# Kernel optimization log

Hardware: AMD Instinct MI355X
Metric: run time of the kernel (lower is better)

The kernel has to match this reference:

```python
import jax, jax.numpy as jnp
import numpy as np

B, T, S = 32, 32, 400
H, E = 512, 300
V, MAX_OOV = 45000, 50
EXT_V = V + MAX_OOV
NEG = 1.0e12  # INF constant from the torch module


def setup_inputs() -> dict:
    key = jax.random.key(0)
    ks = jax.random.split(key, 16)
    p = lambda k, shape: jax.random.normal(k, shape, jnp.float32) * 0.02
    ext = jax.random.randint(ks[0], (B, S), 0, EXT_V, dtype=jnp.int64 if jax.config.jax_enable_x64 else jnp.int32)
    ext = ext.at[0, 0].set(EXT_V - 1)  # pin max OOV id so num_oov == MAX_OOV (matches torch data-dependent size)
    return {
        "trg_seq_embedded": jax.random.normal(ks[1], (B, T, E), jnp.float32),
        "ext_src_seq": ext,
        "init_states": jax.random.normal(ks[2], (1, B, H), jnp.float32),
        "encoder_outputs": jax.random.normal(ks[3], (B, S, H), jnp.float32),
        "encoder_mask": jnp.ones((B, S), jnp.int32),
        "W_enc": p(ks[4], (H, H)), "b_enc": jnp.zeros((H,), jnp.float32),
        "W_red": p(ks[5], (E, E + H)), "b_red": jnp.zeros((E,), jnp.float32),
        "W_ih": p(ks[6], (4 * H, E)), "W_hh": p(ks[7], (4 * H, H)),
        "b_ih": jnp.zeros((4 * H,), jnp.float32), "b_hh": jnp.zeros((4 * H,), jnp.float32),
        "W_cat": p(ks[8], (H, 2 * H)), "b_cat": jnp.zeros((H,), jnp.float32),
        "W_log": p(ks[9], (V, H)), "b_log": jnp.zeros((V,), jnp.float32),
    }


def reference(trg_seq_embedded, ext_src_seq, init_states, encoder_outputs, encoder_mask,
              W_enc, b_enc, W_red, b_red, W_ih, W_hh, b_ih, b_hh, W_cat, b_cat, W_log, b_log):
    batch = trg_seq_embedded.shape[0]
    # encoder features (memories): [B, S, H]
    memories = jnp.einsum('bsh,gh->bsg', encoder_outputs, W_enc) + b_enc
    batch_idx = jnp.arange(batch)[:, None]
    bias = b_ih + b_hh

    def step(carry, emb):
        h, c, ctx, cov = carry
        # reduce_layer on [embedded ; prev_context] -> [B, E]
        x = jnp.concatenate([emb, ctx], axis=-1) @ W_red.T + b_red
        # single-layer LSTM cell, torch gate order i,f,g,o
        gates = x @ W_ih.T + h @ W_hh.T + bias
        i_g, f_g, g_g, o_g = jnp.split(gates, 4, axis=-1)
        c_new = jax.nn.sigmoid(f_g) * c + jax.nn.sigmoid(i_g) * jnp.tanh(g_g)
        h_new = jax.nn.sigmoid(o_g) * jnp.tanh(c_new)
        # Bahdanau-style dot attention
        energy = jnp.einsum('bh,bsh->bs', h_new, memories)
        energy = jnp.where(encoder_mask == 0, -NEG, energy)
        attn = jax.nn.softmax(energy, axis=1)
        context = jnp.einsum('bs,bsh->bh', attn, memories)
        # output projection
        logit_in = jnp.tanh(jnp.concatenate([h_new, context], axis=-1) @ W_cat.T + b_cat)
        logit = logit_in @ W_log.T + b_log  # [B, V]
        # pointer: scatter_max of energies into extended vocabulary
        ext_logit = jnp.concatenate([logit, jnp.zeros((batch, EXT_V - V), logit.dtype)], axis=1)
        out = jnp.full((batch, EXT_V), -NEG, logit.dtype).at[batch_idx, ext_src_seq].max(energy)
        out = jnp.where(out == -NEG, 0.0, out)
        logit2 = ext_logit + out
        logit2 = jnp.where(logit2 == 0.0, -NEG, logit2)
        return (h_new, c_new, context, cov + attn), (logit2, attn, cov, energy)

    h0 = init_states[0]
    carry0 = (h0, h0, jnp.zeros((batch, memories.shape[-1]), trg_seq_embedded.dtype),
              jnp.zeros((batch, memories.shape[1]), trg_seq_embedded.dtype))
    _, (logits, attn_out, cov_out, energies) = jax.lax.scan(
        step, carry0, jnp.swapaxes(trg_seq_embedded, 0, 1))
    # each stacked over time: logits [T,B,EXT_V], attn/coverage/energies [T,B,S]
    return logits, attn_out, cov_out, energies
```

## Files before the change

kernel.cpp:

```cpp
#include <hip/hip_runtime.h>
#include <hip/hip_bf16.h>

typedef _Float16 h2 __attribute__((ext_vector_type(2)));
typedef _Float16 h8 __attribute__((ext_vector_type(8)));
typedef __attribute__((ext_vector_type(4))) float floatx4;

#define NEGF 1.0e12f

#if __has_builtin(__builtin_amdgcn_fdot2)
#define DOT2(a,b,c) __builtin_amdgcn_fdot2((a),(b),(c),false)
#else
static __device__ __forceinline__ float DOT2(h2 a, h2 b, float c){
  return c + (float)a[0]*(float)b[0] + (float)a[1]*(float)b[1];
}
#endif

__device__ __forceinline__ float dot8(h8 a, h8 b, float c){
  h2 a0 = {a[0],a[1]}, a1 = {a[2],a[3]}, a2 = {a[4],a[5]}, a3 = {a[6],a[7]};
  h2 b0 = {b[0],b[1]}, b1 = {b[2],b[3]}, b2 = {b[4],b[5]}, b3 = {b[6],b[7]};
  c = DOT2(a0,b0,c); c = DOT2(a1,b1,c); c = DOT2(a2,b2,c); c = DOT2(a3,b3,c);
  return c;
}

__device__ __forceinline__ unsigned f16bits(float x){
  union { _Float16 h; unsigned short u; } cv; cv.h = (_Float16)x; return (unsigned)cv.u;
}

#define GLD_LDS16(g, l) __builtin_amdgcn_global_load_lds( \
    (const __attribute__((address_space(1))) void*)(g),   \
    (__attribute__((address_space(3))) void*)(l), 16, 0, 0)

#define ALOAD64(p)    __hip_atomic_load((p), __ATOMIC_RELAXED, __HIP_MEMORY_SCOPE_AGENT)
#define ALOAD32(p)    __hip_atomic_load((p), __ATOMIC_RELAXED, __HIP_MEMORY_SCOPE_AGENT)
#define ASTORE32(p,v) __hip_atomic_store((p), (v), __ATOMIC_RELAXED, __HIP_MEMORY_SCOPE_AGENT)

template<int EPI>
__global__ __launch_bounds__(256) void gemm_f16(
    const _Float16* __restrict__ A, const _Float16* __restrict__ B,
    float* __restrict__ Cf, _Float16* __restrict__ Ch,
    const float* __restrict__ bias, int N, int K, int ldc, int ntn)
{
  __shared__ char smem[32768];
  _Float16* Al = (_Float16*)smem;
  _Float16* Bl = (_Float16*)(smem + 16384);
  int bid = blockIdx.x;
  int bn = bid % ntn, bm = bid / ntn;
  int t = threadIdx.x;
  int w = t >> 6, l = t & 63;

  floatx4 acc[4][4];
#pragma unroll
  for (int i = 0; i < 4; ++i)
#pragma unroll
    for (int j = 0; j < 4; ++j) acc[i][j] = (floatx4){0.f, 0.f, 0.f, 0.f};

  const char* Ab = (const char*)A + (size_t)bm * 128 * K * 2;
  const char* Bb = (const char*)B + (size_t)bn * 128 * K * 2;
  const int rowb = K * 2;
  const int r0 = t >> 3;
  const int cbyte = ((t & 7) * 16) ^ (((t >> 3) & 7) << 4);
  char* AlB = (char*)Al;
  char* BlB = (char*)Bl;
  const int wm = (w >> 1) * 64, wn = (w & 1) * 64;

  for (int kt = 0; kt < K; kt += 64) {
    __syncthreads();
#pragma unroll
    for (int c = 0; c < 4; ++c) {
      int row = c * 32 + r0;
      GLD_LDS16(Ab + (size_t)row * rowb + kt * 2 + cbyte, AlB + c * 4096 + t * 16);
      GLD_LDS16(Bb + (size_t)row * rowb + kt * 2 + cbyte, BlB + c * 4096 + t * 16);
    }
    __syncthreads();
#pragma unroll
    for (int kk = 0; kk < 64; kk += 32) {
      h8 af[4], bfv[4];
#pragma unroll
      for (int i = 0; i < 4; ++i) {
        int ra = wm + i * 16 + (l & 15);
        int cb = ((kk << 1) + ((l >> 4) << 4)) ^ ((ra & 7) << 4);
        af[i] = *(const h8*)(AlB + ra * 128 + cb);
      }
#pragma unroll
      for (int j = 0; j < 4; ++j) {
        int ra = wn + j * 16 + (l & 15);
        int cb = ((kk << 1) + ((l >> 4) << 4)) ^ ((ra & 7) << 4);
        bfv[j] = *(const h8*)(BlB + ra * 128 + cb);
      }
#pragma unroll
      for (int i = 0; i < 4; ++i)
#pragma unroll
        for (int j = 0; j < 4; ++j)
          acc[i][j] = __builtin_amdgcn_mfma_f32_16x16x32_f16(af[i], bfv[j], acc[i][j], 0, 0, 0);
    }
  }

  if (EPI == 3) {
    float* Cs = (float*)smem;
#pragma unroll
    for (int half = 0; half < 2; ++half) {
      __syncthreads();
      if ((w >> 1) == half) {
        int rbase = ((l >> 4) << 2);
#pragma unroll
        for (int i = 0; i < 4; ++i)
#pragma unroll
          for (int j = 0; j < 4; ++j)
#pragma unroll
            for (int r = 0; r < 4; ++r)
              Cs[(i * 16 + rbase + r) * 128 + wn + j * 16 + (l & 15)] = acc[i][j][r];
      }
      __syncthreads();
#pragma unroll
      for (int rr = 0; rr < 16; ++rr) {
        int row = rr * 4 + w;
        int grow = bm * 128 + half * 64 + row;
        int cc = bn * 128 + 2 * l;
        float2 v = *(float2*)&Cs[row * 128 + 2 * l];
        float vv0, vv1;
        if (cc < N)     { float x0 = v.x + bias[cc];     vv0 = (x0 == 0.f) ? -NEGF : x0; } else vv0 = -NEGF;
        if (cc + 1 < N) { float x1 = v.y + bias[cc + 1]; vv1 = (x1 == 0.f) ? -NEGF : x1; } else vv1 = -NEGF;
        float* orow = Cf + (size_t)grow * ldc;
        if (cc + 1 < ldc) { float2 o; o.x = vv0; o.y = vv1; *(float2*)(orow + cc) = o; }
        else if (cc < ldc) orow[cc] = vv0;
      }
    }
  } else {
    int mbase = bm * 128 + wm + ((l >> 4) << 2);
    int nbase = bn * 128 + wn + (l & 15);
#pragma unroll
    for (int j = 0; j < 4; ++j) {
      int col = nbase + j * 16;
#pragma unroll
      for (int i = 0; i < 4; ++i) {
#pragma unroll
        for (int r = 0; r < 4; ++r) {
          int row = mbase + i * 16 + r;
          float v = acc[i][j][r];
          if (col < N) {
            float bv = bias ? bias[col] : 0.f;
            if (EPI == 0)      Cf[(size_t)row * ldc + col] = v + bv;
            else if (EPI == 1) Ch[(size_t)row * ldc + col] = (_Float16)(v + bv);
            else               Ch[(size_t)row * ldc + col] = (_Float16)tanhf(v + bv);
          }
        }
      }
    }
  }
}

__global__ void cast_pad_kernel(const float* __restrict__ src, _Float16* __restrict__ dst,
                                int R, int C, int ld_src, int Cpad, int ld_dst, long total){
  long i = (long)blockIdx.x * 256 + threadIdx.x;
  if (i >= total) return;
  int r = (int)(i / Cpad), c = (int)(i % Cpad);
  float v = (r < R && c < C) ? src[(size_t)r * ld_src + c] : 0.f;
  dst[(size_t)r * ld_dst + c] = (_Float16)v;
}

__global__ void cast_emb_kernel(const float* __restrict__ trg, _Float16* __restrict__ dst){
  int i = blockIdx.x * 256 + threadIdx.x;
  if (i >= 1024 * 320) return;
  int m = i / 320, e = i % 320;
  int tt = m >> 5, b = m & 31;
  float v = (e < 300) ? trg[((size_t)b * 32 + tt) * 300 + e] : 0.f;
  dst[i] = (_Float16)v;
}

__global__ void cast_wr2t_kernel(const float* __restrict__ wred, _Float16* __restrict__ dst){
  int i = blockIdx.x * 256 + threadIdx.x;
  if (i >= 512 * 320) return;
  int h = i / 320, e = i % 320;
  float v = (e < 300) ? wred[(size_t)e * 812 + 300 + h] : 0.f;
  dst[i] = (_Float16)v;
}

__global__ void init_kernel(const float* __restrict__ h0, const float* __restrict__ b_ih,
                            const float* __restrict__ b_hh,
                            _Float16* __restrict__ HCzT, float* __restrict__ bias_sum,
                            _Float16* __restrict__ X1h, unsigned* __restrict__ bar){
  int i = blockIdx.x * 256 + threadIdx.x;
  if (i < 32768) {
    int unit = i >> 3, pos = i & 7;
    int kc = unit >> 5, b = unit & 31;
    int k = kc * 8 + pos;
    HCzT[i] = (k < 512) ? (_Float16)h0[b * 512 + k] : (_Float16)0.f;
  }
  if (i < 2048)  bias_sum[i] = b_ih[i] + b_hh[i];
  if (i < 327680) X1h[i] = (_Float16)0.f;
  if (i < 1024) bar[i] = 0u;
}

__device__ __forceinline__ void gbar(unsigned* flags, unsigned gen){
  asm volatile("s_waitcnt vmcnt(0)" ::: "memory");
  __syncthreads();
  if (threadIdx.x == 0) {
    ASTORE32(flags + blockIdx.x, gen);
    for (;;) {
      bool done = true;
#pragma unroll
      for (int i = 0; i < 32; ++i)
        done &= (ALOAD32(flags + i) >= gen);
      if (done) break;
      __builtin_amdgcn_s_sleep(4);
    }
  }
  __syncthreads();
  asm volatile("" ::: "memory");
}

__global__ __launch_bounds__(512, 1) void fused_loop(
    const _Float16* __restrict__ memh, _Float16* __restrict__ HCzT,
    _Float16* __restrict__ HC_A, const _Float16* __restrict__ Wz,
    const float* __restrict__ P, const float* __restrict__ inits,
    const int* __restrict__ mask, float* __restrict__ e_out,
    float* __restrict__ a_out, float* __restrict__ c_out, unsigned* __restrict__ bar)
{
  __shared__ char smem[32768];
  __shared__ __align__(16) float es[400];
  __shared__ float red[16];
  __shared__ float cum[400];
  __shared__ _Float16 hh[512];

  float* gl = (float*)smem;
  const int q = blockIdx.x, t = threadIdx.x;
  const int w = t >> 6, l = t & 63;
  const int mw = w >> 2, nw = w & 3;

  if (t < 400) cum[t] = 0.f;

  float creg = inits[(t >> 4) * 512 + q * 16 + (t & 15)];
  const _Float16* mb = memh + (size_t)q * 400 * 512;

  const _Float16* wbase[4];
#pragma unroll
  for (int s = 0; s < 4; ++s)
    wbase[s] = Wz + (size_t)(s * 512 + q * 16 + (l & 15)) * 1024 + nw * 256 + ((l >> 4) << 3);

  __syncthreads();

  for (int ts = 0; ts < 32; ++ts) {
    {
      unsigned long long* zsrc = (unsigned long long*)(HCzT + (size_t)ts * 32768);
      floatx4 acc[4];
#pragma unroll
      for (int s = 0; s < 4; ++s) acc[s] = (floatx4){0.f, 0.f, 0.f, 0.f};
#pragma unroll
      for (int kk8 = 0; kk8 < 8; ++kk8) {
        int unit = ((nw * 8 + kk8) * 4 + (l >> 4)) * 32 + mw * 16 + (l & 15);
        union { unsigned long long u[2]; h8 v; } za;
        za.u[0] = ALOAD64(zsrc + (size_t)unit * 2);
        za.u[1] = ALOAD64(zsrc + (size_t)unit * 2 + 1);
#pragma unroll
        for (int s = 0; s < 4; ++s) {
          h8 wv = *(const h8*)(wbase[s] + kk8 * 32);
          acc[s] = __builtin_amdgcn_mfma_f32_16x16x32_f16(za.v, wv, acc[s], 0, 0, 0);
        }
      }
#pragma unroll
      for (int s = 0; s < 4; ++s)
#pragma unroll
        for (int r = 0; r < 4; ++r) {
          int b = mw * 16 + ((l >> 4) << 2) + r;
          gl[(s * 4 + nw) * 512 + b * 16 + (l & 15)] = acc[s][r];
        }
    }
    __syncthreads();
    {
      int b = t >> 4, j16 = t & 15;
      const float* Pr = P + ((size_t)ts * 32 + b) * 2048 + q * 16 + j16;
      float g4[4];
#pragma unroll
      for (int s = 0; s < 4; ++s)
        g4[s] = gl[(s * 4 + 0) * 512 + t] + gl[(s * 4 + 1) * 512 + t]
              + gl[(s * 4 + 2) * 512 + t] + gl[(s * 4 + 3) * 512 + t] + Pr[s * 512];
      float ig = 1.f / (1.f + expf(-g4[0]));
      float fg = 1.f / (1.f + expf(-g4[1]));
      float og = 1.f / (1.f + expf(-g4[3]));
      float cn = fg * creg + ig * tanhf(g4[2]);
      float hn = og * tanhf(cn);
      creg = cn;
      unsigned hu = f16bits(hn);
      unsigned other = __shfl_xor(hu, 1);
      if (!(t & 1)) {
        unsigned pack = hu | (other << 16);
        int j = q * 16 + j16;
        unsigned* dst = (unsigned*)((char*)(HCzT + (size_t)(ts + 1) * 32768)
                                    + (((j >> 3) * 32 + b) << 4) + ((j & 7) << 1));
        ASTORE32(dst, pack);
        *(unsigned*)(HC_A + ((size_t)ts * 32 + b) * 1024 + j) = pack;
      }
    }
    gbar(bar, 2 * ts + 1);

    size_t obase = (size_t)ts * 12800 + q * 400;
    {
      if (t < 64) {
        unsigned long long* hsrc = (unsigned long long*)(HCzT + (size_t)(ts + 1) * 32768);
        union { unsigned long long u[2]; h8 v; } ha;
        ha.u[0] = ALOAD64(hsrc + ((size_t)t * 32 + q) * 2);
        ha.u[1] = ALOAD64(hsrc + ((size_t)t * 32 + q) * 2 + 1);
        *(h8*)&hh[t * 8] = ha.v;
      }
      __syncthreads();

      {
        int g = l >> 2, c = l & 3;
#pragma unroll
        for (int r = 0; r < 4; ++r) {
          int sr = r * 16 + g;
          if (sr < 50) {
            int s = w * 50 + sr;
            const _Float16* row = mb + (size_t)s * 512 + c * 128;
            float e = 0.f;
#pragma unroll
            for (int k = 0; k < 16; ++k)
              e = dot8(*(const h8*)(row + k * 8), *(const h8*)&hh[c * 128 + k * 8], e);
            e += __shfl_xor(e, 1);
            e += __shfl_xor(e, 2);
            if (c == 0) {
              if (mask[q * 400 + s] == 0) e = -NEGF;
              es[s] = e;
            }
          }
        }
      }
      __syncthreads();
      if (t < 400) e_out[obase + t] = es[t];

      float v = (t < 400) ? es[t] : -3.4e38f;
      float m = v;
#pragma unroll
      for (int o = 32; o; o >>= 1) m = fmaxf(m, __shfl_xor(m, o));
      if (l == 0) red[w] = m;
      __syncthreads();
      m = red[0];
#pragma unroll
      for (int qq = 1; qq < 8; ++qq) m = fmaxf(m, red[qq]);
      float p = (t < 400) ? expf(v - m) : 0.f;
      float sum = p;
#pragma unroll
      for (int o = 32; o; o >>= 1) sum += __shfl_xor(sum, o);
      if (l == 0) red[8 + w] = sum;
      __syncthreads();
      float tot = red[8];
#pragma unroll
      for (int qq = 9; qq < 16; ++qq) tot += red[qq];
      float inv = 1.f / tot;
      float aval = p * inv;
      if (t < 400) {
        es[t] = aval;
        a_out[obase + t] = aval;
        c_out[obase + t] = cum[t];
        cum[t] += aval;
      }
      __syncthreads();

      float a0 = 0.f, a1 = 0.f, a2 = 0.f, a3 = 0.f;
#pragma unroll 4
      for (int si = 0; si < 400; si += 4) {
        a0 += es[si + 0] * (float)mb[(size_t)(si + 0) * 512 + t];
        a1 += es[si + 1] * (float)mb[(size_t)(si + 1) * 512 + t];
        a2 += es[si + 2] * (float)mb[(size_t)(si + 2) * 512 + t];
        a3 += es[si + 3] * (float)mb[(size_t)(si + 3) * 512 + t];
      }
      float acc2 = (a0 + a1) + (a2 + a3);
      unsigned cu = f16bits(acc2);
      unsigned other = __shfl_xor(cu, 1);
      if (!(t & 1)) {
        unsigned pack = cu | (other << 16);
        int kg = 512 + t;
        unsigned* dst = (unsigned*)((char*)(HCzT + (size_t)(ts + 1) * 32768)
                                    + (((kg >> 3) * 32 + q) << 4) + ((kg & 7) << 1));
        ASTORE32(dst, pack);
        *(unsigned*)(HC_A + ((size_t)ts * 32 + q) * 1024 + kg) = pack;
      }
    }
    gbar(bar, 2 * ts + 2);
  }
}

__global__ __launch_bounds__(512) void pointer_kernel(
    const int* __restrict__ ext, const float* __restrict__ energ, float* __restrict__ logits)
{
  __shared__ int ids[400];
  __shared__ float es[400];
  int tb = blockIdx.x;
  int b = tb & 31;
  int tt = tb >> 5;
  int t = threadIdx.x;
  if (t < 400) {
    ids[t] = ext[b * 400 + t];
    es[t] = energ[(size_t)tt * 12800 + b * 400 + t];
  }
  __syncthreads();
  if (t < 400) {
    int id = ids[t];
    bool first = true;
    for (int s = 0; s < t; ++s) if (ids[s] == id) { first = false; break; }
    if (first) {
      float mx = es[t];
      for (int s = t + 1; s < 400; ++s) if (ids[s] == id) mx = fmaxf(mx, es[s]);
      if (mx != -NEGF) {
        float* p = &logits[(size_t)tb * 45050 + id];
        float base = 0.f;
        if (id < 45000) { float cur = *p; base = (cur == -NEGF) ? 0.f : cur; }
        float nv = base + mx;
        *p = (nv == 0.f) ? -NEGF : nv;
      }
    }
  }
}

extern "C" void kernel_launch(void* const* d_in, const int* in_sizes, int n_in,
                              void* d_out, int out_size, void* d_ws, size_t ws_size,
                              hipStream_t stream) {
  const float* trg   = (const float*)d_in[0];
  const int*   ext   = (const int*)d_in[1];
  const float* inits = (const float*)d_in[2];
  const float* enc   = (const float*)d_in[3];
  const int*   mask  = (const int*)d_in[4];
  const float* W_enc = (const float*)d_in[5];
  const float* b_enc = (const float*)d_in[6];
  const float* W_red = (const float*)d_in[7];
  const float* b_red = (const float*)d_in[8];
  const float* W_ih  = (const float*)d_in[9];
  const float* W_hh  = (const float*)d_in[10];
  const float* b_ih  = (const float*)d_in[11];
  const float* b_hh  = (const float*)d_in[12];
  const float* W_cat = (const float*)d_in[13];
  const float* b_cat = (const float*)d_in[14];
  const float* W_log = (const float*)d_in[15];
  const float* b_log = (const float*)d_in[16];

  float* out = (float*)d_out;
  float* out_logits = out;
  float* out_attn   = out + 46131200;
  float* out_cov    = out_attn + 409600;
  float* out_energy = out_cov + 409600;

  char* ws = (char*)d_ws;
  size_t o = 0;
  auto alloc = [&](size_t bytes) { void* p = ws + o; o += (bytes + 255) & ~(size_t)255; return p; };
  _Float16* mem_h   = (_Float16*)alloc(12800ULL * 512 * 2);
  _Float16* enc_h   = (_Float16*)alloc(12800ULL * 512 * 2);
  _Float16* W_enc_h = (_Float16*)alloc(512ULL * 512 * 2);
  _Float16* emb_h   = (_Float16*)alloc(1024ULL * 320 * 2);
  _Float16* Wr1_h   = (_Float16*)alloc(384ULL * 320 * 2);
  _Float16* X1_h    = (_Float16*)alloc(1024ULL * 320 * 2);
  _Float16* W_ih_h  = (_Float16*)alloc(2048ULL * 320 * 2);
  _Float16* Wr2T_h  = (_Float16*)alloc(512ULL * 320 * 2);
  _Float16* W_cat_h = (_Float16*)alloc(512ULL * 1024 * 2);
  _Float16* W_log_h = (_Float16*)alloc(45056ULL * 512 * 2);
  _Float16* A_log_h = (_Float16*)alloc(1024ULL * 512 * 2);
  _Float16* HCzT    = (_Float16*)alloc(33ULL * 32768 * 2);
  _Float16* HC_A    = (_Float16*)alloc(1024ULL * 1024 * 2);
  _Float16* Wz      = (_Float16*)alloc(2048ULL * 1024 * 2);
  float* P        = (float*)alloc(1024ULL * 2048 * 4);
  float* bias_sum = (float*)alloc(2048ULL * 4);
  unsigned* bar   = (unsigned*)alloc(4096);

  auto blocks = [](long total) { return (int)((total + 255) / 256); };

  init_kernel<<<blocks(327680), 256, 0, stream>>>(inits, b_ih, b_hh, HCzT, bias_sum, X1_h, bar);
  cast_pad_kernel<<<blocks(12800L*512), 256, 0, stream>>>(enc,   enc_h,   12800, 512, 512, 512, 512, 12800L*512);
  cast_pad_kernel<<<blocks(512L*512),   256, 0, stream>>>(W_enc, W_enc_h, 512,   512, 512, 512, 512, 512L*512);
  cast_pad_kernel<<<blocks(384L*320),   256, 0, stream>>>(W_red, Wr1_h,   300,   300, 812, 320, 320, 384L*320);
  cast_pad_kernel<<<blocks(2048L*320),  256, 0, stream>>>(W_ih,  W_ih_h,  2048,  300, 300, 320, 320, 2048L*320);
  cast_pad_kernel<<<blocks(512L*1024),  256, 0, stream>>>(W_cat, W_cat_h, 512,  1024, 1024, 1024, 1024, 512L*1024);
  cast_pad_kernel<<<blocks(45056L*512), 256, 0, stream>>>(W_log, W_log_h, 45000, 512, 512, 512, 512, 45056L*512);
  cast_pad_kernel<<<blocks(2048L*512),  256, 0, stream>>>(W_hh,  Wz,      2048,  512, 512, 512, 1024, 2048L*512);
  cast_emb_kernel<<<blocks(1024L*320), 256, 0, stream>>>(trg, emb_h);
  cast_wr2t_kernel<<<blocks(512L*320), 256, 0, stream>>>(W_red, Wr2T_h);

  gemm_f16<1><<<400, 256, 0, stream>>>(enc_h, W_enc_h, nullptr, mem_h, b_enc, 512, 512, 512, 4);
  gemm_f16<1><<<24,  256, 0, stream>>>(emb_h, Wr1_h, nullptr, X1_h, b_red, 300, 320, 320, 3);
  gemm_f16<0><<<128, 256, 0, stream>>>(X1_h, W_ih_h, P, nullptr, bias_sum, 2048, 320, 2048, 16);
  gemm_f16<1><<<64,  256, 0, stream>>>(W_ih_h, Wr2T_h, nullptr, Wz + 512, nullptr, 512, 320, 1024, 4);

  fused_loop<<<32, 512, 0, stream>>>(mem_h, HCzT, HC_A, Wz, P, inits, mask,
                                     out_energy, out_attn, out_cov, bar);

  gemm_f16<2><<<32, 256, 0, stream>>>(HC_A, W_cat_h, nullptr, A_log_h, b_cat, 512, 1024, 512, 4);
  gemm_f16<3><<<2816, 256, 0, stream>>>(A_log_h, W_log_h, out_logits, nullptr, b_log, 45000, 512, 45050, 352);
  pointer_kernel<<<1024, 512, 0, stream>>>(ext, out_energy, out_logits);
}
```

Baseline: 1.229 ms.

## Double threads per block in fused recurrent loop, split K and attention work

Launches the persistent fused LSTM/attention kernel with 1024 threads instead of 512. The recurrent gate MFMA is split over 8 K-slices instead of 4, with an XOR swizzle on the LDS reduction buffer. Energy rows are spread over 16 waves, and the context reduction splits the source positions in half and combines the halves through shared memory. The barrier spin sleep is also shortened. The aim is to cut per-step latency of the serial recurrence, at the cost of more registers per thread, an extra syncthreads, and a larger partial-sum reduction.

After: 1.612 ms. 1.31x slower.

```diff
diff --git a/kernel.cpp b/kernel.cpp
--- a/kernel.cpp
+++ b/kernel.cpp
@@ -202,40 +202,41 @@
       for (int i = 0; i < 32; ++i)
         done &= (ALOAD32(flags + i) >= gen);
       if (done) break;
-      __builtin_amdgcn_s_sleep(4);
+      __builtin_amdgcn_s_sleep(2);
     }
   }
   __syncthreads();
   asm volatile("" ::: "memory");
 }
 
-__global__ __launch_bounds__(512, 1) void fused_loop(
+__global__ __launch_bounds__(1024, 1) void fused_loop(
     const _Float16* __restrict__ memh, _Float16* __restrict__ HCzT,
     _Float16* __restrict__ HC_A, const _Float16* __restrict__ Wz,
     const float* __restrict__ P, const float* __restrict__ inits,
     const int* __restrict__ mask, float* __restrict__ e_out,
     float* __restrict__ a_out, float* __restrict__ c_out, unsigned* __restrict__ bar)
 {
-  __shared__ char smem[32768];
+  __shared__ float gl[32 * 512];
   __shared__ __align__(16) float es[400];
-  __shared__ float red[16];
+  __shared__ float red[32];
   __shared__ float cum[400];
   __shared__ _Float16 hh[512];
-
-  float* gl = (float*)smem;
+  __shared__ float part[512];
+
   const int q = blockIdx.x, t = threadIdx.x;
   const int w = t >> 6, l = t & 63;
-  const int mw = w >> 2, nw = w & 3;
+  const int mw = w >> 3, nw = w & 7;
 
   if (t < 400) cum[t] = 0.f;
 
-  float creg = inits[(t >> 4) * 512 + q * 16 + (t & 15)];
+  float creg = 0.f;
+  if (t < 512) creg = inits[(t >> 4) * 512 + q * 16 + (t & 15)];
   const _Float16* mb = memh + (size_t)q * 400 * 512;
 
   const _Float16* wbase[4];
 #pragma unroll
   for (int s = 0; s < 4; ++s)
-    wbase[s] = Wz + (size_t)(s * 512 + q * 16 + (l & 15)) * 1024 + nw * 256 + ((l >> 4) << 3);
+    wbase[s] = Wz + (size_t)(s * 512 + q * 16 + (l & 15)) * 1024 + nw * 128 + ((l >> 4) << 3);
 
   __syncthreads();
 
@@ -246,8 +247,8 @@
 #pragma unroll
       for (int s = 0; s < 4; ++s) acc[s] = (floatx4){0.f, 0.f, 0.f, 0.f};
 #pragma unroll
-      for (int kk8 = 0; kk8 < 8; ++kk8) {
-        int unit = ((nw * 8 + kk8) * 4 + (l >> 4)) * 32 + mw * 16 + (l & 15);
+      for (int kk8 = 0; kk8 < 4; ++kk8) {
+        int unit = ((nw * 4 + kk8) * 4 + (l >> 4)) * 32 + mw * 16 + (l & 15);
         union { unsigned long long u[2]; h8 v; } za;
         za.u[0] = ALOAD64(zsrc + (size_t)unit * 2);
         za.u[1] = ALOAD64(zsrc + (size_t)unit * 2 + 1);
@@ -262,18 +263,23 @@
 #pragma unroll
         for (int r = 0; r < 4; ++r) {
           int b = mw * 16 + ((l >> 4) << 2) + r;
-          gl[(s * 4 + nw) * 512 + b * 16 + (l & 15)] = acc[s][r];
+          int idx = (b * 16 + (l & 15)) ^ (((b >> 2) & 1) << 4);
+          gl[(s * 8 + nw) * 512 + idx] = acc[s][r];
         }
     }
     __syncthreads();
-    {
+    if (t < 512) {
       int b = t >> 4, j16 = t & 15;
+      int tsw = t ^ (((t >> 6) & 1) << 4);
       const float* Pr = P + ((size_t)ts * 32 + b) * 2048 + q * 16 + j16;
       float g4[4];
 #pragma unroll
-      for (int s = 0; s < 4; ++s)
-        g4[s] = gl[(s * 4 + 0) * 512 + t] + gl[(s * 4 + 1) * 512 + t]
-              + gl[(s * 4 + 2) * 512 + t] + gl[(s * 4 + 3) * 512 + t] + Pr[s * 512];
+      for (int s = 0; s < 4; ++s) {
+        float acc = 0.f;
+#pragma unroll
+        for (int k = 0; k < 8; ++k) acc += gl[(s * 8 + k) * 512 + tsw];
+        g4[s] = acc + Pr[s * 512];
+      }
       float ig = 1.f / (1.f + expf(-g4[0]));
       float fg = 1.f / (1.f + expf(-g4[1]));
       float og = 1.f / (1.f + expf(-g4[3]));
@@ -307,10 +313,10 @@
       {
         int g = l >> 2, c = l & 3;
 #pragma unroll
-        for (int r = 0; r < 4; ++r) {
+        for (int r = 0; r < 2; ++r) {
           int sr = r * 16 + g;
-          if (sr < 50) {
-            int s = w * 50 + sr;
+          if (sr < 25) {
+            int s = w * 25 + sr;
             const _Float16* row = mb + (size_t)s * 512 + c * 128;
             float e = 0.f;
 #pragma unroll
@@ -336,16 +342,16 @@
       __syncthreads();
       m = red[0];
 #pragma unroll
-      for (int qq = 1; qq < 8; ++qq) m = fmaxf(m, red[qq]);
+      for (int qq = 1; qq < 16; ++qq) m = fmaxf(m, red[qq]);
       float p = (t < 400) ? expf(v - m) : 0.f;
       float sum = p;
 #pragma unroll
       for (int o = 32; o; o >>= 1) sum += __shfl_xor(sum, o);
-      if (l == 0) red[8 + w] = sum;
-      __syncthreads();
-      float tot = red[8];
-#pragma unroll
-      for (int qq = 9; qq < 16; ++qq) tot += red[qq];
+      if (l == 0) red[16 + w] = sum;
+      __syncthreads();
+      float tot = red[16];
+#pragma unroll
+      for (int qq = 17; qq < 32; ++qq) tot += red[qq];
       float inv = 1.f / tot;
       float aval = p * inv;
       if (t < 400) {
@@ -356,24 +362,33 @@
       }
       __syncthreads();
 
-      float a0 = 0.f, a1 = 0.f, a2 = 0.f, a3 = 0.f;
+      {
+        int col = t & 511, half = t >> 9;
+        int s0 = half * 200;
+        float a0 = 0.f, a1 = 0.f, a2 = 0.f, a3 = 0.f;
 #pragma unroll 4
-      for (int si = 0; si < 400; si += 4) {
-        a0 += es[si + 0] * (float)mb[(size_t)(si + 0) * 512 + t];
-        a1 += es[si + 1] * (float)mb[(size_t)(si + 1) * 512 + t];
-        a2 += es[si + 2] * (float)mb[(size_t)(si + 2) * 512 + t];
-        a3 += es[si + 3] * (float)mb[(size_t)(si + 3) * 512 + t];
-      }
-      float acc2 = (a0 + a1) + (a2 + a3);
-      unsigned cu = f16bits(acc2);
-      unsigned other = __shfl_xor(cu, 1);
-      if (!(t & 1)) {
-        unsigned pack = cu | (other << 16);
-        int kg = 512 + t;
-        unsigned* dst = (unsigned*)((char*)(HCzT + (size_t)(ts + 1) * 32768)
-                                    + (((kg >> 3) * 32 + q) << 4) + ((kg & 7) << 1));
-        ASTORE32(dst, pack);
-        *(unsigned*)(HC_A + ((size_t)ts * 32 + q) * 1024 + kg) = pack;
+        for (int si = 0; si < 200; si += 4) {
+          a0 += es[s0 + si + 0] * (float)mb[(size_t)(s0 + si + 0) * 512 + col];
+          a1 += es[s0 + si + 1] * (float)mb[(size_t)(s0 + si + 1) * 512 + col];
+          a2 += es[s0 + si + 2] * (float)mb[(size_t)(s0 + si + 2) * 512 + col];
+          a3 += es[s0 + si + 3] * (float)mb[(size_t)(s0 + si + 3) * 512 + col];
+        }
+        float acc = (a0 + a1) + (a2 + a3);
+        if (half == 0) part[col] = acc;
+        __syncthreads();
+        if (half == 1) {
+          float cv = part[col] + acc;
+          unsigned cu = f16bits(cv);
+          unsigned other = __shfl_xor(cu, 1);
+          if (!(col & 1)) {
+            unsigned pack = cu | (other << 16);
+            int kg = 512 + col;
+            unsigned* dst = (unsigned*)((char*)(HCzT + (size_t)(ts + 1) * 32768)
+                                        + (((kg >> 3) * 32 + q) << 4) + ((kg & 7) << 1));
+            ASTORE32(dst, pack);
+            *(unsigned*)(HC_A + ((size_t)ts * 32 + q) * 1024 + kg) = pack;
+          }
+        }
       }
     }
     gbar(bar, 2 * ts + 2);
@@ -478,8 +493,8 @@
   gemm_f16<0><<<128, 256, 0, stream>>>(X1_h, W_ih_h, P, nullptr, bias_sum, 2048, 320, 2048, 16);
   gemm_f16<1><<<64,  256, 0, stream>>>(W_ih_h, Wr2T_h, nullptr, Wz + 512, nullptr, 512, 320, 1024, 4);
 
-  fused_loop<<<32, 512, 0, stream>>>(mem_h, HCzT, HC_A, Wz, P, inits, mask,
-                                     out_energy, out_attn, out_cov, bar);
+  fused_loop<<<32, 1024, 0, stream>>>(mem_h, HCzT, HC_A, Wz, P, inits, mask,
+                                      out_energy, out_attn, out_cov, bar);
 
   gemm_f16<2><<<32, 256, 0, stream>>>(HC_A, W_cat_h, nullptr, A_log_h, b_cat, 512, 1024, 512, 4);
   gemm_f16<3><<<2816, 256, 0, stream>>>(A_log_h, W_log_h, out_logits, nullptr, b_log, 45000, 512, 45050, 352);
```
